# Kernel tuning notes

Hardware: AMD Instinct MI355X
Metric: run time of the kernel (lower is better)

The kernel has to match this reference:

```python
import jax, jax.numpy as jnp
import numpy as np

N, NS, B = 4096, 256, 2
X, Y, Z = 128, 128, 16
R = 4                      # compress_ratio per spatial axis
C, NC, H = 128, 20, 8      # feat dim, num classes, heads
DH = C // H
EPS = 1e-5


def setup_inputs() -> dict:
    rng = np.random.default_rng(0)
    gx_n, gy_n, gz_n = X // R, Y // R, Z // R
    # pick NS//B unique super-voxel cells per batch element
    cells = np.stack([rng.choice(gx_n * gy_n * gz_n, NS // B, replace=False) for _ in range(B)])
    gx = cells // (gy_n * gz_n)
    rem = cells % (gy_n * gz_n)
    gy, gz = rem // gz_n, rem % gz_n
    bidx = np.repeat(np.arange(B), NS // B)
    sv = np.stack([bidx, gx.ravel(), gy.ravel(), gz.ravel()], axis=1)  # [NS,4]
    per = N // NS  # 16 voxels per super-voxel, distinct offsets in the 4x4x4 cell
    offs = np.argsort(rng.random((NS, R * R * R)), axis=1)[:, :per]
    dx, dy, dz = offs // (R * R), (offs // R) % R, offs % R
    vox = np.stack([
        np.repeat(sv[:, 0], per),
        (sv[:, 1, None] * R + dx).ravel(),
        (sv[:, 2, None] * R + dy).ravel(),
        (sv[:, 3, None] * R + dz).ravel()], axis=1).astype(np.int32)

    ks = jax.random.split(jax.random.key(0), 12)
    p = lambda k, shape, s=0.02: jax.random.normal(k, shape, jnp.float32) * s
    return dict(
        indices=jnp.asarray(vox),
        features=jax.random.normal(ks[0], (N, C), jnp.float32),
        cw1=p(ks[1], (C, C)), cb1=jnp.zeros(C), cg1=jnp.ones(C), cbe1=jnp.zeros(C),
        cw2=p(ks[2], (C, C)), cb2=jnp.zeros(C),
        pw1=p(ks[3], (3, 64)), pb1=jnp.zeros(64), pg1=jnp.ones(64), pbe1=jnp.zeros(64),
        pw2=p(ks[4], (64, 1)), pb2=jnp.zeros(1),
        wq=p(ks[5], (C, C)), bq=jnp.zeros(C),
        wk=p(ks[6], (C, C)), bk=jnp.zeros(C),
        wv=p(ks[7], (C, C)), bv=jnp.zeros(C),
        wo=p(ks[8], (C, C)), bo=jnp.zeros(C),
        ln_g=jnp.ones(C), ln_b=jnp.zeros(C),
        seg_w=p(ks[9], (3, 3, 3, C, NC)), seg_b=jnp.zeros(NC),
    )


def _bn(x, g, b):  # BatchNorm1d, training-mode batch statistics
    mu = x.mean(0)
    var = x.var(0)
    return (x - mu) * jax.lax.rsqrt(var + EPS) * g + b


def reference(indices, features, cw1, cb1, cg1, cbe1, cw2, cb2,
              pw1, pb1, pg1, pbe1, pw2, pb2,
              wq, bq, wk, bk, wv, bv, wo, bo, ln_g, ln_b, seg_w, seg_b):
    ratio = jnp.array([1, R, R, R], dtype=indices.dtype)
    comp = indices // ratio                                  # [N,4] super-voxel coord
    unq, inv = jnp.unique(comp, axis=0, size=NS, return_inverse=True)
    # scatter-add softmax(features) over super-voxels
    cf = jax.ops.segment_sum(jax.nn.softmax(features, axis=1), inv, num_segments=NS)
    h = jax.nn.relu(_bn(cf @ cw1 + cb1, cg1, cbe1)) @ cw2 + cb2      # [NS,C]
    # pairwise relative-position bias: tiny MLP over [N*NS,3]
    pos = (indices[:, None, 1:] - unq[None, :, 1:]).astype(jnp.float32).reshape(N * NS, 3)
    pbias = (jax.nn.relu(_bn(pos @ pw1 + pb1, pg1, pbe1)) @ pw2 + pb2).reshape(N, NS)
    # multi-head cross attention: voxels query super-voxels, bias added to scores
    q = (features @ wq + bq).reshape(N, H, DH)
    k = (h @ wk + bk).reshape(NS, H, DH)
    v = (h @ wv + bv).reshape(NS, H, DH)
    scores = jnp.einsum('nhd,shd->hns', q, k) / np.float32(np.sqrt(DH)) + pbias[None]
    attn = jax.nn.softmax(scores, axis=-1)                   # [H,N,NS]
    ctx = jnp.einsum('hns,shd->nhd', attn, v).reshape(N, C) @ wo + bo
    y = features + ctx                                       # residual + LayerNorm sublayer
    mu = y.mean(-1, keepdims=True)
    var = y.var(-1, keepdims=True)
    y = (y - mu) * jax.lax.rsqrt(var + EPS) * ln_g + ln_b
    # SubMConv3d(128->20, k=3, pad=1): dense scatter -> conv -> gather at active sites
    grid = jnp.zeros((B, X, Y, Z, C), jnp.float32).at[
        indices[:, 0], indices[:, 1], indices[:, 2], indices[:, 3]].set(y)
    out = jax.lax.conv_general_dilated(
        grid, seg_w, (1, 1, 1), 'SAME',
        dimension_numbers=('NDHWC', 'DHWIO', 'NDHWC')) + seg_b
    return out[indices[:, 0], indices[:, 1], indices[:, 2], indices[:, 3]]  # [N,NC]
```

## Files before the change

### kernel.cpp

```cpp
#include <hip/hip_runtime.h>

typedef unsigned short ushort_t;

#define NVOX 4096
#define NSV  256
#define XD   128
#define YD   128
#define ZD   16
#define CD   128
#define NCD  20
#define HD   8
#define DHD  16
#define MAPN 524288
#define EPSF 1e-5f

#define OF_FEAT 0
#define OF_CW1  524288
#define OF_CB1  540672
#define OF_CG1  540800
#define OF_CBE1 540928
#define OF_CW2  541056
#define OF_CB2  557440
#define OF_PW1  557568
#define OF_PB1  557760
#define OF_PG1  557824
#define OF_PBE1 557888
#define OF_PW2  557952
#define OF_PB2  558016
#define OF_WQ   558080
#define OF_BQ   574464
#define OF_WK   574592
#define OF_BK   590976
#define OF_WV   591104
#define OF_BV   607488
#define OF_WO   607616
#define OF_BO   624000
#define OF_LNG  624128
#define OF_LNB  624256
#define OF_SEGW 624384
#define OF_SEGB 693504
#define ARENA_N 693568
#define TOTCVT  624341

__device__ __forceinline__ float bf2f(const ushort_t* p){
  return __uint_as_float(((unsigned)(*p)) << 16);
}
__device__ __forceinline__ ushort_t f2bf(float f){
  unsigned u = __float_as_uint(f);
  u += 0x7fffu + ((u >> 16) & 1u);
  return (ushort_t)(u >> 16);
}
__device__ __forceinline__ float unlo(unsigned u){ return __uint_as_float(u << 16); }
__device__ __forceinline__ float unhi(unsigned u){ return __uint_as_float(u & 0xffff0000u); }

struct SrcPtrs { const void* p[25]; };

__device__ const int g_cnt[25] = {524288,16384,128,128,128,16384,128,192,64,64,64,64,1,
                                  16384,128,16384,128,16384,128,16384,128,128,128,0,20};
__device__ const int g_off[25] = {OF_FEAT,OF_CW1,OF_CB1,OF_CG1,OF_CBE1,OF_CW2,OF_CB2,
                                  OF_PW1,OF_PB1,OF_PG1,OF_PBE1,OF_PW2,OF_PB2,
                                  OF_WQ,OF_BQ,OF_WK,OF_BK,OF_WV,OF_BV,OF_WO,OF_BO,
                                  OF_LNG,OF_LNB,OF_SEGW,OF_SEGB};

__device__ __forceinline__ float ldi(const void* p, int off, int fl){
  return fl ? bf2f((const ushort_t*)p + off) : ((const float*)p)[off];
}

struct SPREP {
  float frows[16][CD];
  float qpart[2][16][CD];
  float part[8][CD];
  float cfs[CD];
  float gpart[8][CD];
};
union __align__(16) UPREP { SPREP sv; int smom[18]; };

__global__ __launch_bounds__(512) void kprep(SrcPtrs sp, const int* idx, int* flag,
    float* arena, float* wt, int* map, float* afold_g, float* scfold_g,
    float* qb, float* t1T)
{
  __shared__ UPREP sm;
  __shared__ int sm_flag;
  int t = threadIdx.x, b = blockIdx.x;
  if (t < 64){
    const ushort_t* f16 = (const ushort_t*)sp.p[0];
    unsigned u = f16[2*t];
    int e = (u >> 7) & 0xFF;
    int sane = (u == 0 || (e >= 90 && e <= 150)) ? 1 : 0;
    unsigned long long bl = __ballot(sane);
    if (t == 0) sm_flag = (__popcll(bl) >= 48) ? 1 : 0;
  }
  __syncthreads();
  const int fl = sm_flag;

  if (b < 255){
    int gid = b*512 + t;
    const int GS = 255*512;
    if (gid == 0) *flag = fl;
    for (int k=gid; k<MAPN; k+=GS) map[k] = -1;
    for (int el=gid; el<TOTCVT; el+=GS){
      int s=0, rem=el;
      while (rem >= g_cnt[s]){ rem -= g_cnt[s]; ++s; }
      arena[g_off[s]+rem] = ldi(sp.p[s], rem, fl);
    }
    for (int k=gid; k<27*NCD*CD; k+=GS){
      int nb = k/(NCD*CD); int rem = k - nb*(NCD*CD); int o = rem/CD, i = rem - o*CD;
      wt[k] = ldi(sp.p[23], nb*(CD*NCD) + i*NCD + o, fl);
    }
  } else if (b < 511){
    int sv = b - 255;
    int rb = sv*16;
    if (fl){
      const uint2* fsrc = (const uint2*)((const ushort_t*)sp.p[0] + (size_t)rb*CD);
      uint2 u = fsrc[t];
      float* dst = &sm.sv.frows[t>>5][(t&31)*4];
      dst[0]=unlo(u.x); dst[1]=unhi(u.x); dst[2]=unlo(u.y); dst[3]=unhi(u.y);
    } else {
      const float4* fsrc = (const float4*)((const float*)sp.p[0] + (size_t)rb*CD);
      ((float4*)sm.sv.frows)[t] = fsrc[t];
    }
    __syncthreads();
    {
      int c8 = (t&15)*8, r = (t>>4)&15, kh = t>>8;
      int i0 = kh*64;
      float acc[8] = {0.f,0.f,0.f,0.f,0.f,0.f,0.f,0.f};
      if (fl){
        const ushort_t* wqp = (const ushort_t*)sp.p[13];
        #pragma unroll 4
        for (int i=i0; i<i0+64; ++i){
          uint4 w4 = *(const uint4*)(wqp + (size_t)i*CD + c8);
          float fr = sm.sv.frows[r][i];
          acc[0] += unlo(w4.x)*fr; acc[1] += unhi(w4.x)*fr;
          acc[2] += unlo(w4.y)*fr; acc[3] += unhi(w4.y)*fr;
          acc[4] += unlo(w4.z)*fr; acc[5] += unhi(w4.z)*fr;
          acc[6] += unlo(w4.w)*fr; acc[7] += unhi(w4.w)*fr;
        }
      } else {
        const float* wqp = (const float*)sp.p[13];
        #pragma unroll 4
        for (int i=i0; i<i0+64; ++i){
          float4 wa = *(const float4*)(wqp + (size_t)i*CD + c8);
          float4 wb = *(const float4*)(wqp + (size_t)i*CD + c8 + 4);
          float fr = sm.sv.frows[r][i];
          acc[0]+=wa.x*fr; acc[1]+=wa.y*fr; acc[2]+=wa.z*fr; acc[3]+=wa.w*fr;
          acc[4]+=wb.x*fr; acc[5]+=wb.y*fr; acc[6]+=wb.z*fr; acc[7]+=wb.w*fr;
        }
      }
      #pragma unroll
      for (int j=0;j<8;++j) sm.sv.qpart[kh][r][c8+j] = acc[j];
    }
    __syncthreads();
    for (int e = t; e < 16*CD; e += 512){
      int r = e>>7, c = e&127;
      qb[(size_t)(rb+r)*CD + c] = sm.sv.qpart[0][r][c] + sm.sv.qpart[1][r][c]
                                + ldi(sp.p[14], c, fl);
    }
    {
      int w = t>>6, l = t&63;
      float a0 = 0.f, a1 = 0.f;
      #pragma unroll
      for (int k=0;k<2;++k){
        int r = w*2 + k;
        float f0 = sm.sv.frows[r][l];
        float f1 = sm.sv.frows[r][l+64];
        float m = fmaxf(f0,f1);
        #pragma unroll
        for (int o=32;o;o>>=1) m = fmaxf(m, __shfl_xor(m,o,64));
        float e0 = __expf(f0-m), e1 = __expf(f1-m);
        float ssum = e0+e1;
        #pragma unroll
        for (int o=32;o;o>>=1) ssum += __shfl_xor(ssum,o,64);
        float inv = 1.f/ssum;
        a0 += e0*inv; a1 += e1*inv;
      }
      sm.sv.part[w][l] = a0; sm.sv.part[w][l+64] = a1;
    }
    __syncthreads();
    if (t < CD){
      float s = 0.f;
      #pragma unroll
      for (int w=0;w<8;++w) s += sm.sv.part[w][t];
      sm.sv.cfs[t] = s;
    }
    __syncthreads();
    {
      int c2 = (t&63)*2, kg = t>>6;
      int i0 = kg*16;
      float a0 = 0.f, a1 = 0.f;
      if (fl){
        const ushort_t* W = (const ushort_t*)sp.p[1];
        #pragma unroll 4
        for (int i=i0; i<i0+16; ++i){
          unsigned w = *(const unsigned*)(W + (size_t)i*CD + c2);
          float cfv = sm.sv.cfs[i];
          a0 += unlo(w)*cfv; a1 += unhi(w)*cfv;
        }
      } else {
        const float* W = (const float*)sp.p[1];
        #pragma unroll 4
        for (int i=i0; i<i0+16; ++i){
          float2 w = *(const float2*)(W + (size_t)i*CD + c2);
          float cfv = sm.sv.cfs[i];
          a0 += w.x*cfv; a1 += w.y*cfv;
        }
      }
      sm.sv.gpart[kg][c2] = a0; sm.sv.gpart[kg][c2+1] = a1;
    }
    __syncthreads();
    if (t < CD){
      float s = 0.f;
      #pragma unroll
      for (int kg=0;kg<8;++kg) s += sm.sv.gpart[kg][t];
      t1T[(size_t)t*NSV + sv] = s + ldi(sp.p[2], t, fl);
    }
  } else {
    if (t < 18) sm.smom[t] = 0;
    __syncthreads();
    {
      int sacc[9] = {0,0,0,0,0,0,0,0,0};
      for (int v = t; v < NVOX; v += 512){
        int4 q = ((const int4*)idx)[v];
        sacc[0]+=q.y; sacc[1]+=q.z; sacc[2]+=q.w;
        sacc[3]+=q.y*q.y; sacc[4]+=q.z*q.z; sacc[5]+=q.w*q.w;
        sacc[6]+=q.y*q.z; sacc[7]+=q.y*q.w; sacc[8]+=q.z*q.w;
      }
      int um[9] = {0,0,0,0,0,0,0,0,0};
      if (t < 256){
        int4 q = ((const int4*)idx)[t*16];
        int gx=q.y>>2, gy=q.z>>2, gz=q.w>>2;
        um[0]=gx; um[1]=gy; um[2]=gz;
        um[3]=gx*gx; um[4]=gy*gy; um[5]=gz*gz;
        um[6]=gx*gy; um[7]=gx*gz; um[8]=gy*gz;
      }
      int lane = t & 63;
      #pragma unroll
      for (int i=0;i<9;++i){
        int s = sacc[i];
        int u = um[i];
        #pragma unroll
        for (int o=32;o;o>>=1){
          s += __shfl_xor(s, o, 64);
          u += __shfl_xor(u, o, 64);
        }
        if (lane == 0){
          if (s) atomicAdd(&sm.smom[9+i], s);
          if (u) atomicAdd(&sm.smom[i], u);
        }
      }
    }
    __syncthreads();
    if (t < 64){
      int* smom = sm.smom;
      double U1[3]={(double)smom[0],(double)smom[1],(double)smom[2]};
      double S1[3]={(double)smom[9],(double)smom[10],(double)smom[11]};
      double Uxx[3][3], Sxx[3][3];
      Uxx[0][0]=smom[3]; Uxx[1][1]=smom[4]; Uxx[2][2]=smom[5];
      Uxx[0][1]=Uxx[1][0]=smom[6]; Uxx[0][2]=Uxx[2][0]=smom[7]; Uxx[1][2]=Uxx[2][1]=smom[8];
      Sxx[0][0]=smom[12]; Sxx[1][1]=smom[13]; Sxx[2][2]=smom[14];
      Sxx[0][1]=Sxx[1][0]=smom[15]; Sxx[0][2]=Sxx[2][0]=smom[16]; Sxx[1][2]=Sxx[2][1]=smom[17];
      double M1[3], M2[3][3];
      for (int a=0;a<3;++a) M1[a] = 256.0*S1[a] - 4096.0*U1[a];
      for (int a=0;a<3;++a)
        for (int b2=0;b2<3;++b2)
          M2[a][b2] = 256.0*Sxx[a][b2] - S1[a]*U1[b2] - S1[b2]*U1[a] + 4096.0*Uxx[a][b2];
      double wv_[3]={(double)ldi(sp.p[7],t,fl),(double)ldi(sp.p[7],64+t,fl),(double)ldi(sp.p[7],128+t,fl)};
      double bj=(double)ldi(sp.p[8],t,fl), gj=(double)ldi(sp.p[9],t,fl), bej=(double)ldi(sp.p[10],t,fl);
      double Mw=0.0, wMw=0.0;
      for (int a=0;a<3;++a){
        Mw += M1[a]*wv_[a];
        for (int b2=0;b2<3;++b2) wMw += wv_[a]*M2[a][b2]*wv_[b2];
      }
      const double NM = 1048576.0;
      double mean = Mw/NM + bj;
      double Ey2  = wMw/NM + 2.0*bj*Mw/NM + bj*bj;
      double var  = Ey2 - mean*mean;
      double scale = gj / sqrt(var + 1e-5);
      afold_g[t]      = (float)(wv_[0]*scale);
      afold_g[64+t]   = (float)(wv_[1]*scale);
      afold_g[128+t]  = (float)(wv_[2]*scale);
      scfold_g[t]     = (float)(bj*scale + bej - mean*scale);
    }
  }
}

__global__ __launch_bounds__(256) void kpb(const float* A, const int* idx,
    const float* afold_g, const float* scfold_g, float* pbias_b)
{
  __shared__ float saf[3][64];
  __shared__ float ssc[64];
  __shared__ float w2s[64];
  __shared__ __align__(16) float e4q[64][8];
  __shared__ float xs[8], ys[8], zs[8];
  int t = threadIdx.x, b = blockIdx.x;
  if (t < 64){
    saf[0][t] = afold_g[t]; saf[1][t] = afold_g[64+t]; saf[2][t] = afold_g[128+t];
    ssc[t] = scfold_g[t]; w2s[t] = A[OF_PW2+t];
  } else if (t < 72){
    int qi = t - 64;
    int4 q = ((const int4*)idx)[b*8 + qi];
    xs[qi] = (float)q.y; ys[qi] = (float)q.z; zs[qi] = (float)q.w;
  }
  __syncthreads();
  for (int e = t; e < 512; e += 256){
    int j = e & 63, qi = e >> 6;
    e4q[j][qi] = saf[0][j]*xs[qi] + saf[1][j]*ys[qi] + saf[2][j]*zs[qi];
  }
  __syncthreads();
  int4 q0 = ((const int4*)idx)[t*16];
  float ux = (float)(q0.y>>2), uy = (float)(q0.z>>2), uz = (float)(q0.w>>2);
  float pb2 = A[OF_PB2];
  float pbv[8];
  #pragma unroll
  for (int i=0;i<8;++i) pbv[i] = pb2;
  #pragma unroll 2
  for (int j=0;j<64;++j){
    float dj = ssc[j] - (saf[0][j]*ux + saf[1][j]*uy + saf[2][j]*uz);
    float wj = w2s[j];
    float4 e0 = *(const float4*)&e4q[j][0];
    float4 e1 = *(const float4*)&e4q[j][4];
    pbv[0] += fmaxf(e0.x+dj,0.f)*wj; pbv[1] += fmaxf(e0.y+dj,0.f)*wj;
    pbv[2] += fmaxf(e0.z+dj,0.f)*wj; pbv[3] += fmaxf(e0.w+dj,0.f)*wj;
    pbv[4] += fmaxf(e1.x+dj,0.f)*wj; pbv[5] += fmaxf(e1.y+dj,0.f)*wj;
    pbv[6] += fmaxf(e1.z+dj,0.f)*wj; pbv[7] += fmaxf(e1.w+dj,0.f)*wj;
  }
  float* dst = pbias_b + ((size_t)b*256 + t)*8;
  *(float4*)dst       = make_float4(pbv[0],pbv[1],pbv[2],pbv[3]);
  *(float4*)(dst + 4) = make_float4(pbv[4],pbv[5],pbv[6],pbv[7]);
}

__global__ __launch_bounds__(256) void k6_fused(const float* t1T, const float* A,
    const int* idx, int* map, float* kb, float* vb){
  __shared__ float row[CD];
  __shared__ float cpar[2][CD];
  __shared__ float hrow[CD];
  int t = threadIdx.x;
  int role = blockIdx.x >> 8, s = blockIdx.x & 255;
  if (role == 0 && t >= 128 && t < 144){
    int v = s*16 + (t-128);
    int4 q = ((const int4*)idx)[v];
    map[((q.x*XD + q.y)*YD + q.z)*ZD + q.w] = v;
  }
  if (t < CD){
    const float4* col = (const float4*)(t1T + (size_t)t*NSV);
    float sum=0.f, sq=0.f;
    #pragma unroll 8
    for (int i=0;i<NSV/4;++i){
      float4 v = col[i];
      sum += v.x+v.y+v.z+v.w;
      sq  += v.x*v.x+v.y*v.y+v.z*v.z+v.w*v.w;
    }
    float mean = sum*(1.f/256.f);
    float var  = sq*(1.f/256.f) - mean*mean;
    float scv = A[OF_CG1+t]*rsqrtf(var+EPSF);
    float shv = A[OF_CBE1+t] - mean*scv;
    row[t] = fmaxf(t1T[(size_t)t*NSV + s]*scv + shv, 0.f);
  }
  __syncthreads();
  int c = t&127, half = t>>7;
  {
    const float* W = A + OF_CW2;
    float acc = 0.f;
    #pragma unroll 8
    for (int i=half*64;i<half*64+64;++i) acc += row[i]*W[i*CD+c];
    cpar[half][c] = acc;
  }
  __syncthreads();
  if (t < CD) hrow[t] = cpar[0][t]+cpar[1][t]+A[OF_CB2+t];
  __syncthreads();
  {
    const float* W = role ? (A+OF_WV) : (A+OF_WK);
    float acc = 0.f;
    #pragma unroll 8
    for (int i=half*64;i<half*64+64;++i) acc += hrow[i]*W[i*CD+c];
    cpar[half][c] = acc;
  }
  __syncthreads();
  if (t < CD){
    float v = cpar[0][t]+cpar[1][t] + (role ? A[OF_BV+t] : A[OF_BK+t]);
    if (role) vb[(size_t)s*CD+t] = v; else kb[(size_t)s*CD+t] = v;
  }
}

#define CGRP(row,hh) (((hh) + ((row)>>1)) & 3)

__global__ __launch_bounds__(256, 6) void k9_attn(
    const float* A, const int* idx, const float* pbias_b,
    const float* kb, const float* vb, const float* qb, float* yb)
{
  __shared__ __align__(16) float q4s[4][CD];
  __shared__ __align__(16) float scf[NSV][16];
  __shared__ __align__(16) float ctxT[CD*4];
  __shared__ float cpart[4][4][64];
  __shared__ float rinv[32];
  int t = threadIdx.x;
  int n0 = blockIdx.x*4;
  if (t < 128) ((float4*)q4s)[t] = ((const float4*)(qb + (size_t)n0*CD))[t];
  float4 pbq = *(const float4*)(pbias_b + ((size_t)(n0>>3)*256 + t)*8 + (n0&7));
  float pbv[4] = {pbq.x, pbq.y, pbq.z, pbq.w};
  __syncthreads();
  const float4* krow = (const float4*)(kb + (size_t)t*CD);
  #pragma unroll
  for (int p=0;p<2;++p){
    {
      #pragma unroll
      for (int hh=0; hh<4; ++hh){
        int h = p*4 + hh;
        float4 k0 = krow[h*4+0], k1 = krow[h*4+1], k2 = krow[h*4+2], k3 = krow[h*4+3];
        float pr[4];
        #pragma unroll
        for (int g=0; g<4; ++g){
          const float* qg = &q4s[g][h*DHD];
          float dot = qg[0]*k0.x + qg[1]*k0.y + qg[2]*k0.z + qg[3]*k0.w
                    + qg[4]*k1.x + qg[5]*k1.y + qg[6]*k1.z + qg[7]*k1.w
                    + qg[8]*k2.x + qg[9]*k2.y + qg[10]*k2.z + qg[11]*k2.w
                    + qg[12]*k3.x + qg[13]*k3.y + qg[14]*k3.z + qg[15]*k3.w;
          pr[g] = __expf(dot*0.25f + pbv[g]);
        }
        *(float4*)&scf[t][CGRP(t,hh)*4] = make_float4(pr[0],pr[1],pr[2],pr[3]);
      }
    }
    __syncthreads();
    {
      int g = t>>6, lane = t&63;
      #pragma unroll
      for (int hh=0; hh<4; ++hh){
        float s0 = 0.f;
        #pragma unroll
        for (int k=0;k<4;++k){
          int r = lane + 64*k;
          s0 += scf[r][CGRP(r,hh)*4 + g];
        }
        #pragma unroll
        for (int o=32;o;o>>=1) s0 += __shfl_xor(s0,o,64);
        if (lane==0) rinv[g*8 + p*4 + hh] = 1.f/s0;
      }
    }
    {
      int q = t>>6, c = t&63;
      int hh = c>>4;
      const float* vcol = vb + p*64 + c;
      float a0=0.f, a1=0.f, a2=0.f, a3=0.f;
      #pragma unroll 4
      for (int s=q*64; s<q*64+64; ++s){
        float v = vcol[(size_t)s*CD];
        float4 pv = *(const float4*)&scf[s][CGRP(s,hh)*4];
        a0 += pv.x*v; a1 += pv.y*v; a2 += pv.z*v; a3 += pv.w*v;
      }
      cpart[q][0][c]=a0; cpart[q][1][c]=a1; cpart[q][2][c]=a2; cpart[q][3][c]=a3;
    }
    __syncthreads();
    {
      int gsel = t>>6, c = t&63;
      int ch = p*64 + c, h = ch>>4;
      ctxT[ch*4+gsel] = (cpart[0][gsel][c]+cpart[1][gsel][c]
                        +cpart[2][gsel][c]+cpart[3][gsel][c]) * rinv[gsel*8+h];
    }
  }
  __syncthreads();
  {
    int half=t>>7, c=t&127;
    const float* wo = A + OF_WO;
    float acc[4]={0.f,0.f,0.f,0.f};
    #pragma unroll 4
    for (int i=half*64;i<half*64+64;++i){
      float wv = wo[i*CD+c];
      float4 r = *(const float4*)&ctxT[i*4];
      acc[0]+=r.x*wv; acc[1]+=r.y*wv; acc[2]+=r.z*wv; acc[3]+=r.w*wv;
    }
    #pragma unroll
    for (int g=0;g<4;++g) cpart[(c>>6)*2 + half][g][c&63] = acc[g];
  }
  __syncthreads();
  if (t < CD){
    float bov = A[OF_BO+t];
    int chi = t>>6, cl = t&63;
    #pragma unroll
    for (int g=0;g<4;++g)
      ctxT[t*4+g] = cpart[chi*2+0][g][cl] + cpart[chi*2+1][g][cl] + bov
                  + A[OF_FEAT + (size_t)(n0+g)*CD + t];
  }
  __syncthreads();
  {
    int g = t>>6, lane = t&63;
    float x0 = ctxT[lane*4+g], x1 = ctxT[(lane+64)*4+g];
    float s1 = x0+x1, s2 = x0*x0+x1*x1;
    #pragma unroll
    for (int o=32;o;o>>=1){ s1 += __shfl_xor(s1,o,64); s2 += __shfl_xor(s2,o,64); }
    float mean = s1*(1.f/128.f);
    float var  = s2*(1.f/128.f) - mean*mean;
    float rs = rsqrtf(var + EPSF);
    yb[(size_t)(n0+g)*CD + lane]    = (x0-mean)*rs*A[OF_LNG+lane]    + A[OF_LNB+lane];
    yb[(size_t)(n0+g)*CD + lane+64] = (x1-mean)*rs*A[OF_LNG+lane+64] + A[OF_LNB+lane+64];
  }
}

__global__ __launch_bounds__(256) void k10_conv(const int* idx, const int* map,
    const float* yb, const float* A, const float* wt, const int* flag, void* outv)
{
  __shared__ int sco4[8][4];
  __shared__ int jn[8][27];
  __shared__ float partial[4][8][NCD];
  int t = threadIdx.x;
  int p0 = blockIdx.x*8;
  if (t < 32) ((int*)sco4)[t] = idx[4*p0 + t];
  __syncthreads();
  if (t < 216){
    int v = t/27, nb = t - v*27;
    int kd = nb/9, kh = (nb/3)%3, kw = nb%3;
    int bb = sco4[v][0];
    int nx = sco4[v][1]+kd-1, ny = sco4[v][2]+kh-1, nz = sco4[v][3]+kw-1;
    int j = -1;
    if ((unsigned)nx < XD && (unsigned)ny < YD && (unsigned)nz < ZD)
      j = map[((bb*XD+nx)*YD+ny)*ZD+nz];
    jn[v][nb] = j;
  }
  __syncthreads();
  int w = t>>6, l = t&63;
  int og = l & 3, cg = l >> 2;
  int c0 = cg*8;
  float acc[8][5];
  #pragma unroll
  for (int v=0;v<8;++v)
    #pragma unroll
    for (int oo=0;oo<5;++oo) acc[v][oo]=0.f;
  for (int nb = w; nb < 27; nb += 4){
    const float* wbase = wt + (size_t)nb*NCD*CD + c0;
    float4 wreg[10];
    #pragma unroll
    for (int oo=0;oo<5;++oo){
      wreg[oo*2]   = *(const float4*)(wbase + (size_t)(og*5+oo)*CD);
      wreg[oo*2+1] = *(const float4*)(wbase + (size_t)(og*5+oo)*CD + 4);
    }
    #pragma unroll
    for (int v=0; v<8; ++v){
      int j = jn[v][nb];
      if (j < 0) continue;
      const float4* y4 = (const float4*)(yb + (size_t)j*CD + c0);
      float4 ya = y4[0], ybb = y4[1];
      #pragma unroll
      for (int oo=0;oo<5;++oo){
        float4 wa = wreg[oo*2], wb = wreg[oo*2+1];
        acc[v][oo] += ya.x*wa.x + ya.y*wa.y + ya.z*wa.z + ya.w*wa.w
                    + ybb.x*wb.x + ybb.y*wb.y + ybb.z*wb.z + ybb.w*wb.w;
      }
    }
  }
  #pragma unroll
  for (int v=0;v<8;++v)
    #pragma unroll
    for (int oo=0;oo<5;++oo){
      float s = acc[v][oo];
      s += __shfl_xor(s, 4, 64);
      s += __shfl_xor(s, 8, 64);
      s += __shfl_xor(s, 16, 64);
      s += __shfl_xor(s, 32, 64);
      if (cg == 0) partial[w][v][og*5+oo] = s;
    }
  __syncthreads();
  if (t < 160){
    int v = t/20, o = t - v*20;
    float s = partial[0][v][o]+partial[1][v][o]+partial[2][v][o]+partial[3][v][o]
            + A[OF_SEGB+o];
    if (*flag) ((ushort_t*)outv)[(size_t)(p0+v)*NCD + o] = f2bf(s);
    else       ((float*)outv)[(size_t)(p0+v)*NCD + o]   = s;
  }
}

extern "C" void kernel_launch(void* const* d_in, const int* in_sizes, int n_in,
                              void* d_out, int out_size, void* d_ws, size_t ws_size,
                              hipStream_t stream) {
  const int* idx = (const int*)d_in[0];

  char* w = (char*)d_ws;
  size_t off = 0;
  #define ALLOC(name, type, count) \
    type* name = (type*)(w + off); off += (((size_t)(count)*sizeof(type)) + 255) & ~(size_t)255;
  ALLOC(flag,   int,   64)
  ALLOC(arena,  float, ARENA_N)
  ALLOC(wt,     float, 27*NCD*CD)
  ALLOC(map,    int,   MAPN)
  ALLOC(afold,  float, 192)
  ALLOC(scfold, float, 64)
  ALLOC(t1T,    float, CD*NSV)
  ALLOC(kb,     float, NSV*CD)
  ALLOC(vbuf,   float, NSV*CD)
  ALLOC(qb,     float, NVOX*CD)
  ALLOC(yb,     float, NVOX*CD)
  ALLOC(pbias_b,float, 512*256*8)
  #undef ALLOC
  (void)off; (void)ws_size; (void)n_in; (void)in_sizes; (void)out_size;

  SrcPtrs sp;
  for (int i=0;i<25;++i) sp.p[i] = d_in[i+1];

  kprep   <<<512, 512, 0, stream>>>(sp, idx, flag, arena, wt, map, afold, scfold, qb, t1T);
  kpb     <<<512, 256, 0, stream>>>(arena, idx, afold, scfold, pbias_b);
  k6_fused<<<NSV*2, 256, 0, stream>>>(t1T, arena, idx, map, kb, vbuf);
  k9_attn <<<NVOX/4, 256, 0, stream>>>(arena, idx, pbias_b, kb, vbuf, qb, yb);
  k10_conv<<<NVOX/8, 256, 0, stream>>>(idx, map, yb, arena, wt, flag, d_out);
}
```

Before: 208.4 us.

## Merge positional-bias and K/V kernels, skip feature arena copy, vectorize q loads

Combines the positional-bias kernel and the K/V projection kernel into one launch with 1024 blocks, dispatching on block index, so one kernel launch and one dependency point go away. The prep kernel no longer copies the 524K-element feature tensor into the fp32 arena. The attention kernel now reads the residual features straight from the source buffer, converting from bf16 when the flag is set. The q·k dot product loads q through float4 shared-memory reads. In exchange, every thread of k9 reads the dtype flag, and the residual read becomes a bf16 gather. Other kernels must not read OF_FEAT from the arena any more.

```diff
diff --git a/kernel.cpp b/kernel.cpp
--- a/kernel.cpp
+++ b/kernel.cpp
@@ -40,7 +40,7 @@
 #define OF_SEGW 624384
 #define OF_SEGB 693504
 #define ARENA_N 693568
-#define TOTCVT  624341
+#define TOTCVT2 100053
 
 __device__ __forceinline__ float bf2f(const ushort_t* p){
   return __uint_as_float(((unsigned)(*p)) << 16);
@@ -55,12 +55,12 @@
 
 struct SrcPtrs { const void* p[25]; };
 
-__device__ const int g_cnt[25] = {524288,16384,128,128,128,16384,128,192,64,64,64,64,1,
-                                  16384,128,16384,128,16384,128,16384,128,128,128,0,20};
-__device__ const int g_off[25] = {OF_FEAT,OF_CW1,OF_CB1,OF_CG1,OF_CBE1,OF_CW2,OF_CB2,
-                                  OF_PW1,OF_PB1,OF_PG1,OF_PBE1,OF_PW2,OF_PB2,
-                                  OF_WQ,OF_BQ,OF_WK,OF_BK,OF_WV,OF_BV,OF_WO,OF_BO,
-                                  OF_LNG,OF_LNB,OF_SEGW,OF_SEGB};
+__device__ const int g_cnt2[24] = {16384,128,128,128,16384,128,192,64,64,64,64,1,
+                                   16384,128,16384,128,16384,128,16384,128,128,128,0,20};
+__device__ const int g_off2[24] = {OF_CW1,OF_CB1,OF_CG1,OF_CBE1,OF_CW2,OF_CB2,
+                                   OF_PW1,OF_PB1,OF_PG1,OF_PBE1,OF_PW2,OF_PB2,
+                                   OF_WQ,OF_BQ,OF_WK,OF_BK,OF_WV,OF_BV,OF_WO,OF_BO,
+                                   OF_LNG,OF_LNB,OF_SEGW,OF_SEGB};
 
 __device__ __forceinline__ float ldi(const void* p, int off, int fl){
   return fl ? bf2f((const ushort_t*)p + off) : ((const float*)p)[off];
@@ -98,10 +98,10 @@
     const int GS = 255*512;
     if (gid == 0) *flag = fl;
     for (int k=gid; k<MAPN; k+=GS) map[k] = -1;
-    for (int el=gid; el<TOTCVT; el+=GS){
+    for (int el=gid; el<TOTCVT2; el+=GS){
       int s=0, rem=el;
-      while (rem >= g_cnt[s]){ rem -= g_cnt[s]; ++s; }
-      arena[g_off[s]+rem] = ldi(sp.p[s], rem, fl);
+      while (rem >= g_cnt2[s]){ rem -= g_cnt2[s]; ++s; }
+      arena[g_off2[s]+rem] = ldi(sp.p[s+1], rem, fl);
     }
     for (int k=gid; k<27*NCD*CD; k+=GS){
       int nb = k/(NCD*CD); int rem = k - nb*(NCD*CD); int o = rem/CD, i = rem - o*CD;
@@ -283,7 +283,8 @@
   }
 }
 
-__global__ __launch_bounds__(256) void kpb(const float* A, const int* idx,
+__global__ __launch_bounds__(256) void k6pb(const float* t1T, const float* A,
+    const int* idx, int* map, float* kb, float* vb,
     const float* afold_g, const float* scfold_g, float* pbias_b)
 {
   __shared__ float saf[3][64];
@@ -291,50 +292,48 @@
   __shared__ float w2s[64];
   __shared__ __align__(16) float e4q[64][8];
   __shared__ float xs[8], ys[8], zs[8];
-  int t = threadIdx.x, b = blockIdx.x;
-  if (t < 64){
-    saf[0][t] = afold_g[t]; saf[1][t] = afold_g[64+t]; saf[2][t] = afold_g[128+t];
-    ssc[t] = scfold_g[t]; w2s[t] = A[OF_PW2+t];
-  } else if (t < 72){
-    int qi = t - 64;
-    int4 q = ((const int4*)idx)[b*8 + qi];
-    xs[qi] = (float)q.y; ys[qi] = (float)q.z; zs[qi] = (float)q.w;
-  }
-  __syncthreads();
-  for (int e = t; e < 512; e += 256){
-    int j = e & 63, qi = e >> 6;
-    e4q[j][qi] = saf[0][j]*xs[qi] + saf[1][j]*ys[qi] + saf[2][j]*zs[qi];
-  }
-  __syncthreads();
-  int4 q0 = ((const int4*)idx)[t*16];
-  float ux = (float)(q0.y>>2), uy = (float)(q0.z>>2), uz = (float)(q0.w>>2);
-  float pb2 = A[OF_PB2];
-  float pbv[8];
-  #pragma unroll
-  for (int i=0;i<8;++i) pbv[i] = pb2;
-  #pragma unroll 2
-  for (int j=0;j<64;++j){
-    float dj = ssc[j] - (saf[0][j]*ux + saf[1][j]*uy + saf[2][j]*uz);
-    float wj = w2s[j];
-    float4 e0 = *(const float4*)&e4q[j][0];
-    float4 e1 = *(const float4*)&e4q[j][4];
-    pbv[0] += fmaxf(e0.x+dj,0.f)*wj; pbv[1] += fmaxf(e0.y+dj,0.f)*wj;
-    pbv[2] += fmaxf(e0.z+dj,0.f)*wj; pbv[3] += fmaxf(e0.w+dj,0.f)*wj;
-    pbv[4] += fmaxf(e1.x+dj,0.f)*wj; pbv[5] += fmaxf(e1.y+dj,0.f)*wj;
-    pbv[6] += fmaxf(e1.z+dj,0.f)*wj; pbv[7] += fmaxf(e1.w+dj,0.f)*wj;
-  }
-  float* dst = pbias_b + ((size_t)b*256 + t)*8;
-  *(float4*)dst       = make_float4(pbv[0],pbv[1],pbv[2],pbv[3]);
-  *(float4*)(dst + 4) = make_float4(pbv[4],pbv[5],pbv[6],pbv[7]);
-}
-
-__global__ __launch_bounds__(256) void k6_fused(const float* t1T, const float* A,
-    const int* idx, int* map, float* kb, float* vb){
   __shared__ float row[CD];
   __shared__ float cpar[2][CD];
   __shared__ float hrow[CD];
-  int t = threadIdx.x;
-  int role = blockIdx.x >> 8, s = blockIdx.x & 255;
+  int t = threadIdx.x, b = blockIdx.x;
+  if (b < 512){
+    if (t < 64){
+      saf[0][t] = afold_g[t]; saf[1][t] = afold_g[64+t]; saf[2][t] = afold_g[128+t];
+      ssc[t] = scfold_g[t]; w2s[t] = A[OF_PW2+t];
+    } else if (t < 72){
+      int qi = t - 64;
+      int4 q = ((const int4*)idx)[b*8 + qi];
+      xs[qi] = (float)q.y; ys[qi] = (float)q.z; zs[qi] = (float)q.w;
+    }
+    __syncthreads();
+    for (int e = t; e < 512; e += 256){
+      int j = e & 63, qi = e >> 6;
+      e4q[j][qi] = saf[0][j]*xs[qi] + saf[1][j]*ys[qi] + saf[2][j]*zs[qi];
+    }
+    __syncthreads();
+    int4 q0 = ((const int4*)idx)[t*16];
+    float ux = (float)(q0.y>>2), uy = (float)(q0.z>>2), uz = (float)(q0.w>>2);
+    float pb2 = A[OF_PB2];
+    float pbv[8];
+    #pragma unroll
+    for (int i=0;i<8;++i) pbv[i] = pb2;
+    #pragma unroll 2
+    for (int j=0;j<64;++j){
+      float dj = ssc[j] - (saf[0][j]*ux + saf[1][j]*uy + saf[2][j]*uz);
+      float wj = w2s[j];
+      float4 e0 = *(const float4*)&e4q[j][0];
+      float4 e1 = *(const float4*)&e4q[j][4];
+      pbv[0] += fmaxf(e0.x+dj,0.f)*wj; pbv[1] += fmaxf(e0.y+dj,0.f)*wj;
+      pbv[2] += fmaxf(e0.z+dj,0.f)*wj; pbv[3] += fmaxf(e0.w+dj,0.f)*wj;
+      pbv[4] += fmaxf(e1.x+dj,0.f)*wj; pbv[5] += fmaxf(e1.y+dj,0.f)*wj;
+      pbv[6] += fmaxf(e1.z+dj,0.f)*wj; pbv[7] += fmaxf(e1.w+dj,0.f)*wj;
+    }
+    float* dst = pbias_b + ((size_t)b*256 + t)*8;
+    *(float4*)dst       = make_float4(pbv[0],pbv[1],pbv[2],pbv[3]);
+    *(float4*)(dst + 4) = make_float4(pbv[4],pbv[5],pbv[6],pbv[7]);
+    return;
+  }
+  int role = (b - 512) >> 8, s = (b - 512) & 255;
   if (role == 0 && t >= 128 && t < 144){
     int v = s*16 + (t-128);
     int4 q = ((const int4*)idx)[v];
@@ -385,7 +384,8 @@
 
 __global__ __launch_bounds__(256, 6) void k9_attn(
     const float* A, const int* idx, const float* pbias_b,
-    const float* kb, const float* vb, const float* qb, float* yb)
+    const float* kb, const float* vb, const float* qb,
+    const void* featsrc, const int* flag, float* yb)
 {
   __shared__ __align__(16) float q4s[4][CD];
   __shared__ __align__(16) float scf[NSV][16];
@@ -394,6 +394,7 @@
   __shared__ float rinv[32];
   int t = threadIdx.x;
   int n0 = blockIdx.x*4;
+  const int fl = *flag;
   if (t < 128) ((float4*)q4s)[t] = ((const float4*)(qb + (size_t)n0*CD))[t];
   float4 pbq = *(const float4*)(pbias_b + ((size_t)(n0>>3)*256 + t)*8 + (n0&7));
   float pbv[4] = {pbq.x, pbq.y, pbq.z, pbq.w};
@@ -409,11 +410,12 @@
         float pr[4];
         #pragma unroll
         for (int g=0; g<4; ++g){
-          const float* qg = &q4s[g][h*DHD];
-          float dot = qg[0]*k0.x + qg[1]*k0.y + qg[2]*k0.z + qg[3]*k0.w
-                    + qg[4]*k1.x + qg[5]*k1.y + qg[6]*k1.z + qg[7]*k1.w
-                    + qg[8]*k2.x + qg[9]*k2.y + qg[10]*k2.z + qg[11]*k2.w
-                    + qg[12]*k3.x + qg[13]*k3.y + qg[14]*k3.z + qg[15]*k3.w;
+          const float4* qg4 = (const float4*)&q4s[g][h*DHD];
+          float4 qa = qg4[0], qbv = qg4[1], qc = qg4[2], qd = qg4[3];
+          float dot = qa.x*k0.x + qa.y*k0.y + qa.z*k0.z + qa.w*k0.w
+                    + qbv.x*k1.x + qbv.y*k1.y + qbv.z*k1.z + qbv.w*k1.w
+                    + qc.x*k2.x + qc.y*k2.y + qc.z*k2.z + qc.w*k2.w
+                    + qd.x*k3.x + qd.y*k3.y + qd.z*k3.z + qd.w*k3.w;
           pr[g] = __expf(dot*0.25f + pbv[g]);
         }
         *(float4*)&scf[t][CGRP(t,hh)*4] = make_float4(pr[0],pr[1],pr[2],pr[3]);
@@ -475,9 +477,11 @@
     float bov = A[OF_BO+t];
     int chi = t>>6, cl = t&63;
     #pragma unroll
-    for (int g=0;g<4;++g)
-      ctxT[t*4+g] = cpart[chi*2+0][g][cl] + cpart[chi*2+1][g][cl] + bov
-                  + A[OF_FEAT + (size_t)(n0+g)*CD + t];
+    for (int g=0;g<4;++g){
+      float fv = fl ? bf2f((const ushort_t*)featsrc + (size_t)(n0+g)*CD + t)
+                    : ((const float*)featsrc)[(size_t)(n0+g)*CD + t];
+      ctxT[t*4+g] = cpart[chi*2+0][g][cl] + cpart[chi*2+1][g][cl] + bov + fv;
+    }
   }
   __syncthreads();
   {
@@ -594,8 +598,7 @@
   for (int i=0;i<25;++i) sp.p[i] = d_in[i+1];
 
   kprep   <<<512, 512, 0, stream>>>(sp, idx, flag, arena, wt, map, afold, scfold, qb, t1T);
-  kpb     <<<512, 256, 0, stream>>>(arena, idx, afold, scfold, pbias_b);
-  k6_fused<<<NSV*2, 256, 0, stream>>>(t1T, arena, idx, map, kb, vbuf);
-  k9_attn <<<NVOX/4, 256, 0, stream>>>(arena, idx, pbias_b, kb, vbuf, qb, yb);
+  k6pb    <<<1024, 256, 0, stream>>>(t1T, arena, idx, map, kb, vbuf, afold, scfold, pbias_b);
+  k9_attn <<<NVOX/4, 256, 0, stream>>>(arena, idx, pbias_b, kb, vbuf, qb, d_in[1], flag, yb);
   k10_conv<<<NVOX/8, 256, 0, stream>>>(idx, map, yb, arena, wt, flag, d_out);
 }
```

Measured after the change: 200.7 us. 1.04x faster.
